# Performance work log

Measured on AMD Instinct MI355X. Metric: run time of the kernel, lower is better.

Reference implementation:

```python
import jax, jax.numpy as jnp
import numpy as np

# --- config (matches init_kwargs) ---
HID = 2048      # hidden_size
H = 16          # num_attention_heads
D_NOPE = 128    # qk_nope_head_dim
D_ROPE = 64     # qk_rope_head_dim
D_Q = D_NOPE + D_ROPE  # 192
D_V = 128       # v_head_dim
QR = 1536       # q_lora_rank
KVR = 512       # kv_lora_rank
PH = 16         # pattern_heads
PD = HID // PH  # 128
THETA = 10000.0
EPS = 1e-6


def rmsnorm(x, w):
    var = jnp.mean(jnp.square(x), axis=-1, keepdims=True)
    return x * jax.lax.rsqrt(var + EPS) * w


def rope_cos_sin(seq_len):
    inv_freq = 1.0 / (THETA ** (jnp.arange(0, D_ROPE, 2, dtype=jnp.float32) / D_ROPE))
    t = jnp.arange(seq_len, dtype=jnp.float32)
    freqs = jnp.outer(t, inv_freq)            # [S, D_ROPE/2]
    emb = jnp.concatenate([freqs, freqs], -1)  # [S, D_ROPE]
    return jnp.cos(emb), jnp.sin(emb)


def rotate_half(x):
    x1, x2 = jnp.split(x, 2, axis=-1)
    return jnp.concatenate([-x2, x1], axis=-1)


def apply_rope(x, cos, sin):
    # x: [B, H, S, D_ROPE]; cos/sin: [S, D_ROPE]
    return x * cos[None, None] + rotate_half(x) * sin[None, None]


def setup_inputs() -> dict:
    key = jax.random.key(0)
    ks = jax.random.split(key, 12)
    def w(k, shape):
        return (jax.random.normal(k, shape, jnp.float32) / np.sqrt(shape[-1])).astype(jnp.float32)
    B, S = 2, 1024
    return {
        "hidden_states": jax.random.normal(ks[0], (B, S, HID), jnp.float32),
        "q_a_w": w(ks[1], (QR, HID)),
        "q_a_ln_w": jnp.ones((QR,), jnp.float32),
        "q_b_w": w(ks[2], (H * D_Q, QR)),
        "kv_a_w": w(ks[3], (KVR + H * D_ROPE, HID)),
        "kv_a_ln_w": jnp.ones((KVR,), jnp.float32),
        "kv_b_w": w(ks[4], (H * (D_NOPE + D_V), KVR)),
        "o_w": w(ks[5], (HID, H * D_V)),
        "sp_q_w": w(ks[6], (HID, HID)),
        "sp_k_w": w(ks[7], (HID, HID)),
        "sp_v_w": w(ks[8], (HID, HID)),
        "sp_o_w": w(ks[9], (HID, HID)),
        "gate_w": w(ks[10], (2, HID)),
        "gate_b": jnp.zeros((2,), jnp.float32),
    }


def reference(hidden_states, q_a_w, q_a_ln_w, q_b_w, kv_a_w, kv_a_ln_w, kv_b_w,
              o_w, sp_q_w, sp_k_w, sp_v_w, sp_o_w, gate_w, gate_b):
    b, s, _ = hidden_states.shape
    dt = hidden_states.dtype

    # ---- main MLA path ----
    q_mid = rmsnorm(hidden_states @ q_a_w.T, q_a_ln_w)                      # [B,S,QR]
    q = (q_mid @ q_b_w.T).reshape(b, s, H, D_Q).transpose(0, 2, 1, 3)       # [B,H,S,Dq]
    q_nope, q_pe = q[..., :D_NOPE], q[..., D_NOPE:]

    kv_a = hidden_states @ kv_a_w.T                                         # [B,S,KVR+H*Dr]
    kv_lora, k_pe_flat = kv_a[..., :KVR], kv_a[..., KVR:]
    k_pe = k_pe_flat.reshape(b, s, H, D_ROPE).transpose(0, 2, 1, 3)         # [B,H,S,Dr]

    kv = (rmsnorm(kv_lora, kv_a_ln_w) @ kv_b_w.T)
    kv = kv.reshape(b, s, H, D_NOPE + D_V).transpose(0, 2, 1, 3)            # [B,H,S,Dn+Dv]
    k_nope, v = kv[..., :D_NOPE], kv[..., D_NOPE:]

    cos, sin = rope_cos_sin(s)
    q_pe = apply_rope(q_pe, cos, sin)
    k_pe = apply_rope(k_pe, cos, sin)

    qf = jnp.concatenate([q_nope, q_pe], -1)                                # [B,H,S,Dq]
    kf = jnp.concatenate([k_nope, k_pe], -1)

    scale = D_Q ** -0.5
    scores = jnp.einsum('bhqd,bhkd->bhqk', qf, kf) * scale
    probs = jax.nn.softmax(scores.astype(jnp.float32), axis=-1).astype(dt)
    ctx = jnp.einsum('bhqk,bhkd->bhqd', probs, v)                           # [B,H,S,Dv]
    main_out = ctx.transpose(0, 2, 1, 3).reshape(b, s, H * D_V) @ o_w.T     # [B,S,HID]

    # ---- self pattern path (standard MHA on hidden_states) ----
    def split_heads(x):
        return x.reshape(b, s, PH, PD).transpose(0, 2, 1, 3)
    pq = split_heads(hidden_states @ sp_q_w.T)
    pk = split_heads(hidden_states @ sp_k_w.T)
    pv = split_heads(hidden_states @ sp_v_w.T)
    p_scores = jnp.einsum('bhqd,bhkd->bhqk', pq, pk) * (PD ** -0.5)
    p_probs = jax.nn.softmax(p_scores.astype(jnp.float32), axis=-1).astype(dt)
    p_ctx = jnp.einsum('bhqk,bhkd->bhqd', p_probs, pv)
    pattern_out = p_ctx.transpose(0, 2, 1, 3).reshape(b, s, HID) @ sp_o_w.T

    # ---- learned gate over paths ----
    gates = jax.nn.softmax(hidden_states @ gate_w.T + gate_b, axis=-1)      # [B,S,2]
    return gates[..., 0:1] * main_out + gates[..., 1:2] * pattern_out
```

## Files before the change

kernel.cpp:

```cpp
#include <hip/hip_runtime.h>
#include <math.h>
#include <stdint.h>

#define HIDN  2048
#define NH    16
#define DNOPE 128
#define DROPE 64
#define DQ    192
#define DV    128
#define QRANK 1536
#define KVRANK 512
#define SEQ   1024
#define NBATCH 2
#define NTOK  (NBATCH*SEQ)
#define EPSV  1e-6f

typedef unsigned short u16;
typedef unsigned int   u32;
typedef __attribute__((ext_vector_type(8))) short  short8;
typedef __attribute__((ext_vector_type(8))) unsigned short ushort8;
typedef __attribute__((ext_vector_type(4))) float  f32x4;

__device__ __forceinline__ u16 f2b(float f) {
    u32 u = __float_as_uint(f);
    u = (u + 0x7fffu + ((u >> 16) & 1u)) >> 16;
    return (u16)u;
}
__device__ __forceinline__ float b2f(u16 h) {
    return __uint_as_float(((u32)h) << 16);
}

__device__ __forceinline__ void async_copy16(const u16* g, u16* l) {
    __builtin_amdgcn_global_load_lds(
        (const __attribute__((address_space(1))) u32*)g,
        (__attribute__((address_space(3))) u32*)l,
        16, 0, 0);
}

__device__ __forceinline__ int swz(int r, int c) { return r * 4 + (c ^ ((r >> 1) & 3)); }

#define DPP_ROR(x, ctrl) __int_as_float(__builtin_amdgcn_update_dpp( \
    __float_as_int(x), __float_as_int(x), ctrl, 0xF, 0xF, false))

__device__ __forceinline__ float rowmax16(float x) {
    x = fmaxf(x, DPP_ROR(x, 0x121));
    x = fmaxf(x, DPP_ROR(x, 0x122));
    x = fmaxf(x, DPP_ROR(x, 0x124));
    x = fmaxf(x, DPP_ROR(x, 0x128));
    return x;
}
__device__ __forceinline__ float rowsum16(float x) {
    x += DPP_ROR(x, 0x121);
    x += DPP_ROR(x, 0x122);
    x += DPP_ROR(x, 0x124);
    x += DPP_ROR(x, 0x128);
    return x;
}

struct CastArgs {
    const float* s[10];
    u16* d[10];
    int cum[11];
    const float* lnq;
    const float* lnkv;
};
__global__ __launch_bounds__(256)
void cast_all(CastArgs a, int total_chunks)
{
    int c = blockIdx.x * 256 + threadIdx.x;
    if (c >= total_chunks) return;
    int seg = 0;
    #pragma unroll
    for (int i = 1; i < 10; ++i) seg += (c >= a.cum[i]) ? 1 : 0;
    int local = c - a.cum[seg];
    const float* src = a.s[seg] + (size_t)local * 8;
    u16* dst = a.d[seg] + (size_t)local * 8;
    float4 x = *(const float4*)(src);
    float4 y = *(const float4*)(src + 4);
    if (seg == 3 || seg == 4) {
        const float* ln = (seg == 3) ? a.lnq : a.lnkv;
        u32 kmod = (seg == 3) ? (u32)QRANK : (u32)KVRANK;
        u32 kb = ((u32)local * 8u) % kmod;
        float4 w0 = *(const float4*)(ln + kb);
        float4 w1 = *(const float4*)(ln + kb + 4);
        x.x *= w0.x; x.y *= w0.y; x.z *= w0.z; x.w *= w0.w;
        y.x *= w1.x; y.y *= w1.y; y.z *= w1.z; y.w *= w1.w;
    }
    ushort8 o;
    o[0]=f2b(x.x); o[1]=f2b(x.y); o[2]=f2b(x.z); o[3]=f2b(x.w);
    o[4]=f2b(y.x); o[5]=f2b(y.y); o[6]=f2b(y.z); o[7]=f2b(y.w);
    *(ushort8*)(dst) = o;
}

struct GemmSeg {
    const u16* X; const u16* W;
    float* Cf; u16* Cb; u16* Cb2; u16* Cb3;
    int K; int ldx; int ldc; int mode; int bx0;
};
struct GemmArgs { GemmSeg seg[3]; int nseg; float* ssq; float* sskv;
                  const float2* gates; };

__global__ __launch_bounds__(256)
void gemm_multi(GemmArgs a)
{
    __shared__ __align__(16) u16 As[2 * 4096];
    __shared__ __align__(16) u16 Bs[2 * 4096];
    int s = 0;
    if (a.nseg > 1 && (int)blockIdx.y >= a.seg[1].bx0) s = 1;
    if (a.nseg > 2 && (int)blockIdx.y >= a.seg[2].bx0) s = 2;
    const GemmSeg g = a.seg[s];

    const int tid = threadIdx.x;
    const int bn = ((int)blockIdx.y - g.bx0) * 128;
    const int bm = blockIdx.x * 128;
    const int lane = tid & 63, wv = tid >> 6;
    const int lm = lane & 15, lq = lane >> 4;
    const int wm = (wv >> 1) * 64, wn = (wv & 1) * 64;
    const int ldx = g.ldx, K = g.K;
    const u16* Xp = g.X;
    const u16* Wp = g.W;

    auto stage = [&](int kt, int buf) {
        int k0 = kt * 32;
        #pragma unroll
        for (int it = 0; it < 2; ++it) {
            int base = wv * 64 + it * 256;
            int slot = base + lane;
            int r = slot >> 2, c = (slot & 3) ^ ((r >> 1) & 3);
            async_copy16(Xp + (size_t)(bm + r) * ldx + k0 + c * 8,
                         As + buf * 4096 + base * 8);
            async_copy16(Wp + (size_t)(bn + r) * K + k0 + c * 8,
                         Bs + buf * 4096 + base * 8);
        }
    };

    f32x4 acc[4][4] = {};
    const int niter = K >> 5;
    stage(0, 0);
    for (int kt = 0; kt < niter; ++kt) {
        int cur = kt & 1;
        __syncthreads();
        if (kt + 1 < niter) stage(kt + 1, cur ^ 1);
        const u16* Ab = As + cur * 4096;
        const u16* Bb = Bs + cur * 4096;
        short8 af[4], bf[4];
        #pragma unroll
        for (int mt = 0; mt < 4; ++mt) {
            int R = wm + mt * 16 + lm;
            af[mt] = *(const short8*)(Ab + swz(R, lq) * 8);
        }
        #pragma unroll
        for (int nt = 0; nt < 4; ++nt) {
            int R = wn + nt * 16 + lm;
            bf[nt] = *(const short8*)(Bb + swz(R, lq) * 8);
        }
        #pragma unroll
        for (int mt = 0; mt < 4; ++mt)
            #pragma unroll
            for (int nt = 0; nt < 4; ++nt)
                acc[mt][nt] = __builtin_amdgcn_mfma_f32_16x16x32_bf16(
                    af[mt], bf[nt], acc[mt][nt], 0, 0, 0);
    }

    const int mode = g.mode;
    if (mode == 1) {
        const int h2  = (bn + wn) / DQ;
        const int hd0 = (bn + wn) % DQ;
        const bool ropeH = (hd0 == 128);
        float invf0 = 0.f, invf1 = 0.f;
        if (ropeH) {
            invf0 = exp2f((float)lm * -0.41524101186f);
            invf1 = exp2f((float)(16 + lm) * -0.41524101186f);
        }
        #pragma unroll
        for (int mt = 0; mt < 4; ++mt) {
            int token0 = bm + wm + mt * 16 + lq * 4;
            #pragma unroll
            for (int i = 0; i < 4; ++i) {
                int tok = token0 + i;
                int b2 = tok >> 10, s2 = tok & (SEQ - 1);
                float inv = rsqrtf(a.ssq[tok] * (1.f / QRANK) + EPSV);
                u16* row = g.Cb + ((size_t)((b2 * NH + h2) * SEQ + s2)) * DQ + hd0;
                if (!ropeH) {
                    #pragma unroll
                    for (int nt = 0; nt < 4; ++nt)
                        row[nt * 16 + lm] = f2b(acc[mt][nt][i] * inv);
                } else {
                    float sn0, c0, sn1, c1;
                    sincosf((float)s2 * invf0, &sn0, &c0);
                    sincosf((float)s2 * invf1, &sn1, &c1);
                    float x10 = acc[mt][0][i] * inv, x20 = acc[mt][2][i] * inv;
                    float x11 = acc[mt][1][i] * inv, x21 = acc[mt][3][i] * inv;
                    row[lm]          = f2b(x10 * c0 - x20 * sn0);
                    row[32 + lm]     = f2b(x20 * c0 + x10 * sn0);
                    row[16 + lm]     = f2b(x11 * c1 - x21 * sn1);
                    row[48 + lm]     = f2b(x21 * c1 + x11 * sn1);
                }
            }
        }
        return;
    }
    #pragma unroll
    for (int mt = 0; mt < 4; ++mt) {
        int token0 = bm + wm + mt * 16 + lq * 4;
        #pragma unroll
        for (int i = 0; i < 4; ++i) {
            int tok = token0 + i;
            int b2 = tok >> 10, s2 = tok & (SEQ - 1);
            float invkv = 1.f, gv = 1.f;
            if (mode == 3) invkv = rsqrtf(a.sskv[tok] * (1.f / KVRANK) + EPSV);
            if (mode == 6) {
                float2 g2 = a.gates[tok];
                gv = (g.ldc == 0) ? g2.x : g2.y;
            }
            #pragma unroll
            for (int nt = 0; nt < 4; ++nt) {
                int feat = bn + wn + nt * 16 + lm;
                float v = acc[mt][nt][i];
                if (mode == 6) {
                    g.Cf[(size_t)tok * HIDN + feat] = gv * v;
                } else if (mode == 5) {
                    g.Cb[(size_t)tok * g.ldc + feat] = f2b(v);
                } else if (mode == 3) {
                    v *= invkv;
                    int h2 = feat >> 8, c = feat & 255;
                    if (c < 128)
                        g.Cb[((size_t)((b2 * NH + h2) * SEQ + s2)) * DQ + c] = f2b(v);
                    else
                        g.Cb2[((size_t)((b2 * NH + h2) * 128 + (c - 128))) * SEQ + s2] = f2b(v);
                } else {
                    int wsel = feat >> 11;
                    int f2 = feat & 2047;
                    int h2 = f2 >> 7, d = f2 & 127;
                    if (wsel == 0)
                        g.Cb[((size_t)((b2 * NH + h2) * SEQ + s2)) * 128 + d] = f2b(v);
                    else if (wsel == 1)
                        g.Cb2[((size_t)((b2 * NH + h2) * SEQ + s2)) * 128 + d] = f2b(v);
                    else
                        g.Cb3[((size_t)((b2 * NH + h2) * 128 + d)) * SEQ + s2] = f2b(v);
                }
            }
        }
    }
    if (mode == 5) {
        float* ssp = nullptr;
        if (bn < QRANK) ssp = a.ssq;
        else if (bn < QRANK + KVRANK) ssp = a.sskv;
        if (ssp) {
            #pragma unroll
            for (int mt = 0; mt < 4; ++mt) {
                int token0 = bm + wm + mt * 16 + lq * 4;
                #pragma unroll
                for (int i = 0; i < 4; ++i) {
                    float sq = 0.f;
                    #pragma unroll
                    for (int nt = 0; nt < 4; ++nt) {
                        float v = acc[mt][nt][i];
                        sq += v * v;
                    }
                    sq = rowsum16(sq);
                    if (lm == 0) atomicAdd(&ssp[token0 + i], sq);
                }
            }
        }
    }
}

__global__ __launch_bounds__(256)
void add_combine(float* __restrict__ out, const float* __restrict__ patout)
{
    const int n4 = NTOK * HIDN / 4;
    for (int i = blockIdx.x * 256 + threadIdx.x; i < n4; i += gridDim.x * 256) {
        float4 o = ((const float4*)out)[i];
        float4 q = ((const float4*)patout)[i];
        o.x += q.x; o.y += q.y; o.z += q.z; o.w += q.w;
        ((float4*)out)[i] = o;
    }
}

__global__ __launch_bounds__(256)
void gate_kern(const float* __restrict__ x, const float* __restrict__ gw,
               const float* __restrict__ gb, float2* __restrict__ gates)
{
    const int tok = blockIdx.x;
    const float* xr = x + (size_t)tok * HIDN;
    float d0 = 0.f, d1 = 0.f;
    for (int i = threadIdx.x; i < HIDN; i += 256) {
        float v = xr[i];
        d0 += v * gw[i];
        d1 += v * gw[HIDN + i];
    }
    __shared__ float r0[256], r1[256];
    r0[threadIdx.x] = d0; r1[threadIdx.x] = d1;
    __syncthreads();
    for (int off = 128; off > 0; off >>= 1) {
        if (threadIdx.x < off) {
            r0[threadIdx.x] += r0[threadIdx.x + off];
            r1[threadIdx.x] += r1[threadIdx.x + off];
        }
        __syncthreads();
    }
    if (threadIdx.x == 0) {
        float l0 = r0[0] + gb[0], l1 = r1[0] + gb[1];
        float m = fmaxf(l0, l1);
        float e0 = __expf(l0 - m), e1 = __expf(l1 - m);
        float inv = 1.f / (e0 + e1);
        gates[tok] = make_float2(e0 * inv, e1 * inv);
    }
}

__global__ __launch_bounds__(256)
void rope_k(const u16* __restrict__ amid, u16* __restrict__ kf)
{
    int t = blockIdx.x * 256 + threadIdx.x;
    int i = t & 31, s = (t >> 5) & (SEQ - 1), bh = t >> 15;
    float inv_freq = exp2f((float)i * -0.41524101186f);
    float ang = (float)s * inv_freq;
    float c, sn; sincosf(ang, &sn, &c);
    int h = bh & (NH - 1), bb = bh >> 4;
    const u16* src = amid + ((size_t)(bb * SEQ + s)) * 3072 + (QRANK + KVRANK) + h * DROPE;
    float x1 = b2f(src[i]), x2 = b2f(src[32 + i]);
    u16* dst = kf + ((size_t)bh * SEQ + s) * DQ + DNOPE;
    dst[i]      = f2b(x1 * c - x2 * sn);
    dst[32 + i] = f2b(x2 * c + x1 * sn);
}

template<int DQK>
__device__ __forceinline__
void flash_body(const u16* __restrict__ Q, const u16* __restrict__ Kf,
                const u16* __restrict__ Vt, u16* __restrict__ ctx_out,
                float scale, u16* Ks, u16* Vs, u16* Ps, int qt, int h, int bb)
{
    constexpr int KSZ  = 32 * DQK;
    constexpr int VSZ  = 32 * 128;
    constexpr int NKIT = DQK / 64;
    constexpr int NT   = SEQ / 32;
    const int tid = threadIdx.x, lane = tid & 63, wv = tid >> 6;
    const int lm = lane & 15, lq = lane >> 4;
    const size_t bh = (size_t)bb * NH + h;
    const u16* Qb = Q + (bh * SEQ + qt * 128 + wv * 32) * (size_t)DQK;
    const u16* Kb = Kf + bh * SEQ * (size_t)DQK;
    const u16* Vb = Vt + bh * (size_t)128 * SEQ;

    short8 qfrag[2][DQK / 32];
    #pragma unroll
    for (int rh = 0; rh < 2; ++rh)
        #pragma unroll
        for (int ks = 0; ks < DQK / 32; ++ks)
            qfrag[rh][ks] = *(const short8*)(Qb + (rh * 16 + lm) * DQK + ks * 32 + lq * 8);

    auto stage = [&](int kt, int buf) {
        #pragma unroll
        for (int it = 0; it < NKIT; ++it) {
            int base = it * 256 + wv * 64;
            int slot = base + lane;
            int plane = slot >> 7, rem = slot & 127;
            int key = rem >> 2, c = (rem & 3) ^ ((key >> 1) & 3);
            async_copy16(Kb + (size_t)(kt * 32 + key) * DQK + plane * 32 + c * 8,
                         Ks + buf * KSZ + base * 8);
        }
        #pragma unroll
        for (int it = 0; it < 2; ++it) {
            int base = it * 256 + wv * 64;
            int slot = base + lane;
            int d = slot >> 2, c = (slot & 3) ^ ((d >> 1) & 3);
            async_copy16(Vb + (size_t)d * SEQ + kt * 32 + c * 8,
                         Vs + buf * VSZ + base * 8);
        }
    };

    float m_i[2][4], l_i[2][4];
    #pragma unroll
    for (int rh = 0; rh < 2; ++rh)
        #pragma unroll
        for (int i = 0; i < 4; ++i) { m_i[rh][i] = -INFINITY; l_i[rh][i] = 0.f; }
    f32x4 oacc[2][8] = {};

    stage(0, 0);
    for (int kt = 0; kt < NT; ++kt) {
        int cur = kt & 1;
        __syncthreads();
        if (kt + 1 < NT) stage(kt + 1, cur ^ 1);
        const u16* Kc = Ks + cur * KSZ;
        const u16* Vc = Vs + cur * VSZ;

        f32x4 sacc[2][2] = {};
        #pragma unroll
        for (int kb = 0; kb < 2; ++kb)
            #pragma unroll
            for (int ks = 0; ks < DQK / 32; ++ks) {
                int R = kb * 16 + lm;
                short8 kfr = *(const short8*)(Kc + ks * 1024 + swz(R, lq) * 8);
                sacc[0][kb] = __builtin_amdgcn_mfma_f32_16x16x32_bf16(
                    qfrag[0][ks], kfr, sacc[0][kb], 0, 0, 0);
                sacc[1][kb] = __builtin_amdgcn_mfma_f32_16x16x32_bf16(
                    qfrag[1][ks], kfr, sacc[1][kb], 0, 0, 0);
            }

        float p0[2][4], p1[2][4], mx[2][4];
        bool needb = false;
        #pragma unroll
        for (int rh = 0; rh < 2; ++rh)
            #pragma unroll
            for (int i = 0; i < 4; ++i) {
                float s0 = sacc[rh][0][i] * scale, s1 = sacc[rh][1][i] * scale;
                float m2 = rowmax16(fmaxf(s0, s1));
                p0[rh][i] = s0; p1[rh][i] = s1; mx[rh][i] = m2;
                needb |= (m2 > m_i[rh][i] + 8.f);
            }
        bool need = __any(needb);
        float alpha[2][4];
        if (need) {
            #pragma unroll
            for (int rh = 0; rh < 2; ++rh)
                #pragma unroll
                for (int i = 0; i < 4; ++i) {
                    float mnew = fmaxf(m_i[rh][i], mx[rh][i]);
                    alpha[rh][i] = __expf(m_i[rh][i] - mnew);
                    m_i[rh][i] = mnew;
                    l_i[rh][i] *= alpha[rh][i];
                }
        }
        #pragma unroll
        for (int rh = 0; rh < 2; ++rh)
            #pragma unroll
            for (int i = 0; i < 4; ++i) {
                p0[rh][i] = __expf(p0[rh][i] - m_i[rh][i]);
                p1[rh][i] = __expf(p1[rh][i] - m_i[rh][i]);
                l_i[rh][i] += rowsum16(p0[rh][i] + p1[rh][i]);
            }

        u16* Pw = Ps + wv * 1280;
        #pragma unroll
        for (int rh = 0; rh < 2; ++rh)
            #pragma unroll
            for (int i = 0; i < 4; ++i) {
                Pw[(rh * 16 + lq * 4 + i) * 40 + lm]      = f2b(p0[rh][i]);
                Pw[(rh * 16 + lq * 4 + i) * 40 + 16 + lm] = f2b(p1[rh][i]);
            }
        short8 pfrag0 = *(const short8*)(Pw + lm * 40 + lq * 8);
        short8 pfrag1 = *(const short8*)(Pw + (16 + lm) * 40 + lq * 8);

        if (need) {
            #pragma unroll
            for (int rh = 0; rh < 2; ++rh)
                #pragma unroll
                for (int nt = 0; nt < 8; ++nt)
                    #pragma unroll
                    for (int i = 0; i < 4; ++i) oacc[rh][nt][i] *= alpha[rh][i];
        }
        #pragma unroll
        for (int nt = 0; nt < 8; ++nt) {
            int R = nt * 16 + lm;
            short8 vfr = *(const short8*)(Vc + swz(R, lq) * 8);
            oacc[0][nt] = __builtin_amdgcn_mfma_f32_16x16x32_bf16(
                pfrag0, vfr, oacc[0][nt], 0, 0, 0);
            oacc[1][nt] = __builtin_amdgcn_mfma_f32_16x16x32_bf16(
                pfrag1, vfr, oacc[1][nt], 0, 0, 0);
        }
    }

    #pragma unroll
    for (int rh = 0; rh < 2; ++rh) {
        int s0 = qt * 128 + wv * 32 + rh * 16 + lq * 4;
        #pragma unroll
        for (int i = 0; i < 4; ++i) {
            float inv = 1.f / l_i[rh][i];
            u16* dst = ctx_out + ((size_t)(bb * SEQ + s0 + i) * NH + h) * 128;
            #pragma unroll
            for (int nt = 0; nt < 8; ++nt)
                dst[nt * 16 + lm] = f2b(oacc[rh][nt][i] * inv);
        }
    }
}

__global__ __launch_bounds__(256, 2)
void flash_fused(const u16* qf, const u16* kf, const u16* Vtg, u16* ctx,
                 const u16* pq, const u16* pk, const u16* pvt, u16* p_ctx,
                 float scale_main, float scale_pat)
{
    __shared__ __align__(16) u16 Ks[2 * 32 * DQ];
    __shared__ __align__(16) u16 Vs[2 * 32 * 128];
    __shared__ __align__(16) u16 Ps[4 * 32 * 40];
    int h = blockIdx.x, qtb = blockIdx.y, bb = blockIdx.z;
    if (qtb < 8)
        flash_body<DQ>(qf, kf, Vtg, ctx, scale_main, Ks, Vs, Ps, qtb, h, bb);
    else
        flash_body<128>(pq, pk, pvt, p_ctx, scale_pat, Ks, Vs, Ps, qtb - 8, h, bb);
}

extern "C" void kernel_launch(void* const* d_in, const int* in_sizes, int n_in,
                              void* d_out, int out_size, void* d_ws, size_t ws_size,
                              hipStream_t stream)
{
    const float* X        = (const float*)d_in[0];
    const float* q_a_w    = (const float*)d_in[1];
    const float* q_a_ln_w = (const float*)d_in[2];
    const float* q_b_w    = (const float*)d_in[3];
    const float* kv_a_w   = (const float*)d_in[4];
    const float* kv_a_ln_w= (const float*)d_in[5];
    const float* kv_b_w   = (const float*)d_in[6];
    const float* o_w      = (const float*)d_in[7];
    const float* sp_q_w   = (const float*)d_in[8];
    const float* sp_k_w   = (const float*)d_in[9];
    const float* sp_v_w   = (const float*)d_in[10];
    const float* sp_o_w   = (const float*)d_in[11];
    const float* gate_w   = (const float*)d_in[12];
    const float* gate_b   = (const float*)d_in[13];
    float* out = (float*)d_out;

    char* p = (char*)d_ws;
    auto alloc = [&](size_t bytes) -> char* {
        char* r = p; p += (bytes + 255) & ~(size_t)255; return r;
    };
    u16* amid      = (u16*)alloc((size_t)NTOK * 3072 * 2);
    u16* Xb        = (u16*)alloc((size_t)NTOK * HIDN * 2);
    u16* aw_b      = (u16*)alloc((size_t)3072 * HIDN * 2);
    u16* q_b_wb    = (u16*)alloc((size_t)NH * DQ * QRANK * 2);
    u16* kv_b_wb   = (u16*)alloc((size_t)NH * 256 * KVRANK * 2);
    u16* o_wb      = (u16*)alloc((size_t)HIDN * HIDN * 2);
    u16* spqkv_wb  = (u16*)alloc((size_t)3 * HIDN * HIDN * 2);
    u16* sp_o_wb   = (u16*)alloc((size_t)HIDN * HIDN * 2);
    u16* qf        = (u16*)alloc((size_t)NTOK * NH * DQ * 2);
    u16* kf        = (u16*)alloc((size_t)NTOK * NH * DQ * 2);
    u16* Vtg       = (u16*)alloc((size_t)NBATCH * NH * 128 * SEQ * 2);
    u16* pq        = (u16*)alloc((size_t)NTOK * HIDN * 2);
    u16* pk        = (u16*)alloc((size_t)NTOK * HIDN * 2);
    float* ssbuf   = (float*)alloc((size_t)2 * NTOK * 4);
    float2* gates  = (float2*)alloc((size_t)NTOK * 8);
    u16* pvt    = aw_b;
    u16* ctx    = q_b_wb;
    u16* p_ctx  = spqkv_wb;
    float* patout = (float*)qf;
    float* ss_q  = ssbuf;
    float* ss_kv = ssbuf + NTOK;

    dim3 blk(256);

    hipMemsetAsync(ssbuf, 0, (size_t)2 * NTOK * 4, stream);

    CastArgs ca;
    const float* srcs[10] = {X, q_a_w, kv_a_w, q_b_w, kv_b_w, o_w,
                             sp_q_w, sp_k_w, sp_v_w, sp_o_w};
    u16* dsts[10] = {Xb, aw_b, aw_b + (size_t)QRANK * HIDN, q_b_wb, kv_b_wb, o_wb,
                     spqkv_wb, spqkv_wb + (size_t)HIDN * HIDN,
                     spqkv_wb + (size_t)2 * HIDN * HIDN, sp_o_wb};
    int ns[10] = {NTOK * HIDN, QRANK * HIDN, 1536 * HIDN, NH * DQ * QRANK,
                  NH * 256 * KVRANK, HIDN * HIDN, HIDN * HIDN, HIDN * HIDN,
                  HIDN * HIDN, HIDN * HIDN};
    int cum = 0;
    for (int i = 0; i < 10; ++i) {
        ca.s[i] = srcs[i]; ca.d[i] = dsts[i];
        ca.cum[i] = cum; cum += ns[i] / 8;
    }
    ca.cum[10] = cum;
    ca.lnq = q_a_ln_w; ca.lnkv = kv_a_ln_w;
    cast_all<<<dim3((cum + 255) / 256), blk, 0, stream>>>(ca, cum);

    gate_kern<<<dim3(NTOK), blk, 0, stream>>>(X, gate_w, gate_b, gates);

    {
        GemmArgs ga = {};
        ga.nseg = 1;
        ga.seg[0] = {Xb, aw_b, nullptr, amid, nullptr, nullptr,
                     HIDN, HIDN, 3072, 5, 0};
        ga.ssq = ss_q; ga.sskv = ss_kv;
        gemm_multi<<<dim3(16, 24), blk, 0, stream>>>(ga);
    }

    {
        GemmArgs ga = {};
        ga.nseg = 3;
        ga.seg[0] = {Xb, spqkv_wb, nullptr, pq, pk, pvt,
                     HIDN, HIDN, 0, 4, 0};
        ga.seg[1] = {amid, q_b_wb, nullptr, qf, nullptr, nullptr,
                     QRANK, 3072, 0, 1, 48};
        ga.seg[2] = {amid + QRANK, kv_b_wb, nullptr, kf, Vtg, nullptr,
                     KVRANK, 3072, 0, 3, 72};
        ga.ssq = ss_q; ga.sskv = ss_kv;
        gemm_multi<<<dim3(16, 104), blk, 0, stream>>>(ga);
    }

    rope_k<<<dim3(4096), blk, 0, stream>>>(amid, kf);

    flash_fused<<<dim3(NH, 16, NBATCH), blk, 0, stream>>>(
        qf, kf, Vtg, ctx, pq, pk, pvt, p_ctx,
        1.0f / sqrtf((float)DQ), 1.0f / sqrtf(128.0f));

    {
        GemmArgs ga = {};
        ga.nseg = 2;
        ga.seg[0] = {ctx, o_wb, out, nullptr, nullptr, nullptr,
                     HIDN, HIDN, 0, 6, 0};
        ga.seg[1] = {p_ctx, sp_o_wb, patout, nullptr, nullptr, nullptr,
                     HIDN, HIDN, 1, 6, 16};
        ga.gates = gates;
        gemm_multi<<<dim3(16, 32), blk, 0, stream>>>(ga);
    }

    add_combine<<<dim3(1024), blk, 0, stream>>>(out, patout);
}
```

Baseline: 526.0 us.

## Fuse K rope into first GEMM epilogue and read V fragments directly from global

The k_pe rope rotation moves into the epilogue of the first projection GEMM, which writes the rotated values straight into kf and drops the separate rope_k kernel and its extra read of amid. In the flash attention kernel, V is no longer staged through shared memory; each wave loads its V fragments directly from global memory every key tile. This cuts LDS use and one kernel launch, but V loads are no longer asynchronous or shared across waves, so each wave repeats the same global reads and may expose memory latency.

```diff
diff --git a/kernel.cpp b/kernel.cpp
--- a/kernel.cpp
+++ b/kernel.cpp
@@ -196,6 +196,31 @@
                     row[16 + lm]     = f2b(x11 * c1 - x21 * sn1);
                     row[48 + lm]     = f2b(x21 * c1 + x11 * sn1);
                 }
+            }
+        }
+        return;
+    }
+    if (mode == 5 && bn >= QRANK + KVRANK) {
+        const int h2 = (bn + wn - (QRANK + KVRANK)) >> 6;
+        float invf0 = exp2f((float)lm * -0.41524101186f);
+        float invf1 = exp2f((float)(16 + lm) * -0.41524101186f);
+        #pragma unroll
+        for (int mt = 0; mt < 4; ++mt) {
+            int token0 = bm + wm + mt * 16 + lq * 4;
+            #pragma unroll
+            for (int i = 0; i < 4; ++i) {
+                int tok = token0 + i;
+                int b2 = tok >> 10, s2 = tok & (SEQ - 1);
+                float sn0, c0, sn1, c1;
+                sincosf((float)s2 * invf0, &sn0, &c0);
+                sincosf((float)s2 * invf1, &sn1, &c1);
+                float x10 = acc[mt][0][i], x20 = acc[mt][2][i];
+                float x11 = acc[mt][1][i], x21 = acc[mt][3][i];
+                u16* row = g.Cb2 + ((size_t)((b2 * NH + h2) * SEQ + s2)) * DQ + DNOPE;
+                row[lm]      = f2b(x10 * c0 - x20 * sn0);
+                row[32 + lm] = f2b(x20 * c0 + x10 * sn0);
+                row[16 + lm] = f2b(x11 * c1 - x21 * sn1);
+                row[48 + lm] = f2b(x21 * c1 + x11 * sn1);
             }
         }
         return;
@@ -243,24 +268,20 @@
         }
     }
     if (mode == 5) {
-        float* ssp = nullptr;
-        if (bn < QRANK) ssp = a.ssq;
-        else if (bn < QRANK + KVRANK) ssp = a.sskv;
-        if (ssp) {
-            #pragma unroll
-            for (int mt = 0; mt < 4; ++mt) {
-                int token0 = bm + wm + mt * 16 + lq * 4;
+        float* ssp = (bn < QRANK) ? a.ssq : a.sskv;
+        #pragma unroll
+        for (int mt = 0; mt < 4; ++mt) {
+            int token0 = bm + wm + mt * 16 + lq * 4;
+            #pragma unroll
+            for (int i = 0; i < 4; ++i) {
+                float sq = 0.f;
                 #pragma unroll
-                for (int i = 0; i < 4; ++i) {
-                    float sq = 0.f;
-                    #pragma unroll
-                    for (int nt = 0; nt < 4; ++nt) {
-                        float v = acc[mt][nt][i];
-                        sq += v * v;
-                    }
-                    sq = rowsum16(sq);
-                    if (lm == 0) atomicAdd(&ssp[token0 + i], sq);
+                for (int nt = 0; nt < 4; ++nt) {
+                    float v = acc[mt][nt][i];
+                    sq += v * v;
                 }
+                sq = rowsum16(sq);
+                if (lm == 0) atomicAdd(&ssp[token0 + i], sq);
             }
         }
     }
@@ -309,30 +330,13 @@
     }
 }
 
-__global__ __launch_bounds__(256)
-void rope_k(const u16* __restrict__ amid, u16* __restrict__ kf)
-{
-    int t = blockIdx.x * 256 + threadIdx.x;
-    int i = t & 31, s = (t >> 5) & (SEQ - 1), bh = t >> 15;
-    float inv_freq = exp2f((float)i * -0.41524101186f);
-    float ang = (float)s * inv_freq;
-    float c, sn; sincosf(ang, &sn, &c);
-    int h = bh & (NH - 1), bb = bh >> 4;
-    const u16* src = amid + ((size_t)(bb * SEQ + s)) * 3072 + (QRANK + KVRANK) + h * DROPE;
-    float x1 = b2f(src[i]), x2 = b2f(src[32 + i]);
-    u16* dst = kf + ((size_t)bh * SEQ + s) * DQ + DNOPE;
-    dst[i]      = f2b(x1 * c - x2 * sn);
-    dst[32 + i] = f2b(x2 * c + x1 * sn);
-}
-
 template<int DQK>
 __device__ __forceinline__
 void flash_body(const u16* __restrict__ Q, const u16* __restrict__ Kf,
                 const u16* __restrict__ Vt, u16* __restrict__ ctx_out,
-                float scale, u16* Ks, u16* Vs, u16* Ps, int qt, int h, int bb)
+                float scale, u16* Ks, u16* Ps, int qt, int h, int bb)
 {
     constexpr int KSZ  = 32 * DQK;
-    constexpr int VSZ  = 32 * 128;
     constexpr int NKIT = DQK / 64;
     constexpr int NT   = SEQ / 32;
     const int tid = threadIdx.x, lane = tid & 63, wv = tid >> 6;
@@ -359,14 +363,6 @@
             async_copy16(Kb + (size_t)(kt * 32 + key) * DQK + plane * 32 + c * 8,
                          Ks + buf * KSZ + base * 8);
         }
-        #pragma unroll
-        for (int it = 0; it < 2; ++it) {
-            int base = it * 256 + wv * 64;
-            int slot = base + lane;
-            int d = slot >> 2, c = (slot & 3) ^ ((d >> 1) & 3);
-            async_copy16(Vb + (size_t)d * SEQ + kt * 32 + c * 8,
-                         Vs + buf * VSZ + base * 8);
-        }
     };
 
     float m_i[2][4], l_i[2][4];
@@ -382,7 +378,11 @@
         __syncthreads();
         if (kt + 1 < NT) stage(kt + 1, cur ^ 1);
         const u16* Kc = Ks + cur * KSZ;
-        const u16* Vc = Vs + cur * VSZ;
+
+        short8 vfr[8];
+        #pragma unroll
+        for (int nt = 0; nt < 8; ++nt)
+            vfr[nt] = *(const short8*)(Vb + (size_t)(nt * 16 + lm) * SEQ + kt * 32 + lq * 8);
 
         f32x4 sacc[2][2] = {};
         #pragma unroll
@@ -451,12 +451,10 @@
         }
         #pragma unroll
         for (int nt = 0; nt < 8; ++nt) {
-            int R = nt * 16 + lm;
-            short8 vfr = *(const short8*)(Vc + swz(R, lq) * 8);
             oacc[0][nt] = __builtin_amdgcn_mfma_f32_16x16x32_bf16(
-                pfrag0, vfr, oacc[0][nt], 0, 0, 0);
+                pfrag0, vfr[nt], oacc[0][nt], 0, 0, 0);
             oacc[1][nt] = __builtin_amdgcn_mfma_f32_16x16x32_bf16(
-                pfrag1, vfr, oacc[1][nt], 0, 0, 0);
+                pfrag1, vfr[nt], oacc[1][nt], 0, 0, 0);
         }
     }
 
@@ -480,13 +478,12 @@
                  float scale_main, float scale_pat)
 {
     __shared__ __align__(16) u16 Ks[2 * 32 * DQ];
-    __shared__ __align__(16) u16 Vs[2 * 32 * 128];
     __shared__ __align__(16) u16 Ps[4 * 32 * 40];
     int h = blockIdx.x, qtb = blockIdx.y, bb = blockIdx.z;
     if (qtb < 8)
-        flash_body<DQ>(qf, kf, Vtg, ctx, scale_main, Ks, Vs, Ps, qtb, h, bb);
+        flash_body<DQ>(qf, kf, Vtg, ctx, scale_main, Ks, Ps, qtb, h, bb);
     else
-        flash_body<128>(pq, pk, pvt, p_ctx, scale_pat, Ks, Vs, Ps, qtb - 8, h, bb);
+        flash_body<128>(pq, pk, pvt, p_ctx, scale_pat, Ks, Ps, qtb - 8, h, bb);
 }
 
 extern "C" void kernel_launch(void* const* d_in, const int* in_sizes, int n_in,
@@ -562,7 +559,7 @@
     {
         GemmArgs ga = {};
         ga.nseg = 1;
-        ga.seg[0] = {Xb, aw_b, nullptr, amid, nullptr, nullptr,
+        ga.seg[0] = {Xb, aw_b, nullptr, amid, kf, nullptr,
                      HIDN, HIDN, 3072, 5, 0};
         ga.ssq = ss_q; ga.sskv = ss_kv;
         gemm_multi<<<dim3(16, 24), blk, 0, stream>>>(ga);
@@ -581,8 +578,6 @@
         gemm_multi<<<dim3(16, 104), blk, 0, stream>>>(ga);
     }
 
-    rope_k<<<dim3(4096), blk, 0, stream>>>(amid, kf);
-
     flash_fused<<<dim3(NH, 16, NBATCH), blk, 0, stream>>>(
         qf, kf, Vtg, ctx, pq, pk, pvt, p_ctx,
         1.0f / sqrtf((float)DQ), 1.0f / sqrtf(128.0f));
```

New measurement: 541.3 us. +2.9%, slower.
